# Optimization experiments

Hardware: AMD Instinct MI355X
Metric: run time of the kernel (lower is better)

The kernel has to match this reference:

```python
import jax, jax.numpy as jnp
import numpy as np

B, S, D, H = 2, 2048, 1024, 16
DK = D // H


def setup_inputs() -> dict:
    key = jax.random.key(0)
    ks = jax.random.split(key, 7)
    q = jax.random.normal(ks[0], (B, S, D), dtype=jnp.float32)
    k = jax.random.normal(ks[1], (B, S, D), dtype=jnp.float32)
    v = jax.random.normal(ks[2], (B, S, D), dtype=jnp.float32)
    # causal mask: mask==0 positions get -1e9 before softmax
    mask = jnp.tril(jnp.ones((S, S), dtype=jnp.int32))[None, None, :, :]
    scale = 0.02
    w_q = jax.random.normal(ks[3], (D, D), dtype=jnp.float32) * scale
    w_k = jax.random.normal(ks[4], (D, D), dtype=jnp.float32) * scale
    w_v = jax.random.normal(ks[5], (D, D), dtype=jnp.float32) * scale
    w_o = jax.random.normal(ks[6], (D, D), dtype=jnp.float32) * scale
    return {"q": q, "k": k, "v": v, "mask": mask,
            "w_q": w_q, "w_k": w_k, "w_v": w_v, "w_o": w_o}


def reference(q, k, v, mask, w_q, w_k, w_v, w_o):
    # nn.Linear(bias=False): x @ W.T
    query = q @ w_q.T  # [B,S,D]
    key = k @ w_k.T
    value = v @ w_v.T
    # split heads -> [B,H,S,DK]
    query = query.reshape(B, S, H, DK).transpose(0, 2, 1, 3)
    key = key.reshape(B, S, H, DK).transpose(0, 2, 1, 3)
    value = value.reshape(B, S, H, DK).transpose(0, 2, 1, 3)
    scores = jnp.einsum('bhqd,bhkd->bhqk', query, key) / jnp.sqrt(
        jnp.asarray(DK, dtype=query.dtype))
    scores = jnp.where(mask == 0, jnp.asarray(-1e9, scores.dtype), scores)
    attn = jax.nn.softmax(scores, axis=-1)  # dropout p=0.0 -> identity
    x = jnp.einsum('bhqk,bhkd->bhqd', attn, value)  # [B,H,S,DK]
    x = x.transpose(0, 2, 1, 3).reshape(B, S, D)
    return x @ w_o.T
```

## Files before the change

### kernel.cpp

```cpp
#include <hip/hip_runtime.h>

typedef __attribute__((ext_vector_type(8))) short short8;
typedef __attribute__((ext_vector_type(4))) float f32x4;

#define DEVI static __device__ __forceinline__

constexpr int BB = 2, SS = 2048, DD = 1024, HH = 16, DKK = 64;
constexpr size_t QN = (size_t)BB * SS * DD;
constexpr size_t WN = (size_t)DD * DD;

constexpr size_t OFF_WQ = 3 * QN;
constexpr size_t OFF_WO = OFF_WQ + 3 * WN;
constexpr size_t OFF_QM = OFF_WQ + 4 * WN;
constexpr size_t OFF_KM = OFF_QM + QN;
constexpr size_t OFF_VM = OFF_QM + 2 * QN;
constexpr size_t OFF_XC = OFF_QM + 3 * QN;

DEVI unsigned short f2bf(float f) {
  unsigned int u = __float_as_uint(f);
  u = (u + 0x7fffu + ((u >> 16) & 1u)) >> 16;
  return (unsigned short)u;
}

DEVI f32x4 fzero() { f32x4 z = {0.f, 0.f, 0.f, 0.f}; return z; }

DEVI void gld16(const void* g, void* l) {
  __builtin_amdgcn_global_load_lds((__attribute__((address_space(1))) void*)g,
                                   (__attribute__((address_space(3))) void*)l,
                                   16, 0, 0);
}

DEVI short8 mk8u(unsigned int a, unsigned int b, unsigned int c, unsigned int d) {
  union { short8 s; unsigned int u[4]; } x;
  x.u[0] = a; x.u[1] = b; x.u[2] = c; x.u[3] = d;
  return x.s;
}

DEVI short8 mk8q(unsigned long long lo, unsigned long long hi) {
  union { short8 s; unsigned long long q[2]; } x;
  x.q[0] = lo; x.q[1] = hi;
  return x.s;
}

DEVI unsigned int pkbf(float a, float b) {
  return __builtin_amdgcn_perm(__float_as_uint(b), __float_as_uint(a), 0x07060302u);
}

#define VMBAR(N) asm volatile("s_waitcnt vmcnt(" #N ")\n\ts_barrier" ::: "memory")
#define LGKM0                                      \
  do {                                             \
    asm volatile("s_waitcnt lgkmcnt(0)" ::: "memory"); \
    __builtin_amdgcn_sched_barrier(0);             \
  } while (0)

__global__ __launch_bounds__(256) void convert_all(
    const float* __restrict__ q, const float* __restrict__ k,
    const float* __restrict__ v, const float* __restrict__ wq,
    const float* __restrict__ wk, const float* __restrict__ wv,
    const float* __restrict__ wo, unsigned short* __restrict__ ws) {
  size_t t = (size_t)blockIdx.x * 256 + threadIdx.x;
  size_t e = t * 4;
  const float* src;
  size_t base, idx;
  if (e < 3 * QN) {
    size_t a = e >> 22;
    idx = e & (QN - 1);
    src = (a == 0) ? q : (a == 1) ? k : v;
    base = a * QN;
  } else {
    size_t r = e - 3 * QN;
    size_t a = r >> 20;
    idx = r & (WN - 1);
    src = (a == 0) ? wq : (a == 1) ? wk : (a == 2) ? wv : wo;
    base = 3 * QN + a * WN;
  }
  float4 f = *(const float4*)(src + idx);
  ushort4 o;
  o.x = f2bf(f.x); o.y = f2bf(f.y); o.z = f2bf(f.z); o.w = f2bf(f.w);
  *(ushort4*)(ws + base + idx) = o;
}

__global__ __launch_bounds__(512, 2) void proj_gemm(unsigned short* __restrict__ ws) {
  __shared__ unsigned short lds[65536];
  const int tid = threadIdx.x;
  const int w = tid >> 6, l = tid & 63;
  const int lr = l & 15, qd = l >> 4, l7 = l & 7, l3 = l >> 3;
  const int wr = w >> 2, wc = w & 3;

  const int orig = blockIdx.x;
  const int swz = (orig & 7) * 24 + (orig >> 3);
  const int mt = swz >> 2, nt = swz & 3;
  const int z = mt >> 4;
  const int m0 = (mt & 15) * 256, n0 = nt * 256;

  const unsigned short* Ab = ws + (size_t)z * QN;
  const unsigned short* Wb = ws + OFF_WQ + (size_t)z * WN;
  unsigned short* O = ws + OFF_QM + (size_t)z * QN;

  f32x4 acc[8][4];
#pragma unroll
  for (int i = 0; i < 8; ++i)
#pragma unroll
    for (int j = 0; j < 4; ++j) acc[i][j] = fzero();

  auto stage = [&](int buf, int ab, int h, int kt) {
    const unsigned short* src = ab ? Wb : Ab;
    const int rc0 = (ab ? n0 : m0) + h * 128 + w * 8 + l3;
    const int kofs = kt * 64 + ((l7 ^ l3) * 8);
    unsigned short* d = &lds[buf * 32768 + ab * 16384 + h * 8192 + w * 512];
#pragma unroll
    for (int u = 0; u < 2; ++u)
      gld16(src + (size_t)(rc0 + u * 64) * DD + kofs, d + u * 4096);
  };
  auto rdA = [&](int buf, int fi, int ks) -> short8 {
    const int rg = (fi * 2 + wr) * 16 + lr;
    const int c2 = (ks * 4 + qd) ^ l7;
    return *(const short8*)&lds[buf * 32768 + rg * 64 + c2 * 8];
  };
  auto rdB = [&](int buf, int fj, int ks) -> short8 {
    const int rg = (fj * 4 + wc) * 16 + lr;
    const int c2 = (ks * 4 + qd) ^ l7;
    return *(const short8*)&lds[buf * 32768 + 16384 + rg * 64 + c2 * 8];
  };

  stage(0, 0, 0, 0);
  stage(0, 1, 0, 0);
  stage(0, 1, 1, 0);
  stage(0, 0, 1, 0);

  constexpr int NT = DD / 64;
#pragma unroll 1
  for (int t = 0; t < NT; ++t) {
    const int rb = t & 1, wb = rb ^ 1;
    const bool g = (t + 1 < NT);
    short8 af[4][2], bf[2][2], bh[2][2];

    VMBAR(4);
    if (g) stage(wb, 0, 0, t + 1);
#pragma unroll
    for (int mi = 0; mi < 4; ++mi)
#pragma unroll
      for (int ks = 0; ks < 2; ++ks) af[mi][ks] = rdA(rb, mi, ks);
#pragma unroll
    for (int nj = 0; nj < 2; ++nj)
#pragma unroll
      for (int ks = 0; ks < 2; ++ks) bf[nj][ks] = rdB(rb, nj, ks);
    LGKM0;
    __builtin_amdgcn_s_setprio(1);
#pragma unroll
    for (int mi = 0; mi < 4; ++mi)
#pragma unroll
      for (int nj = 0; nj < 2; ++nj)
#pragma unroll
        for (int ks = 0; ks < 2; ++ks)
          acc[mi][nj] = __builtin_amdgcn_mfma_f32_16x16x32_bf16(
              af[mi][ks], bf[nj][ks], acc[mi][nj], 0, 0, 0);
    __builtin_amdgcn_s_setprio(0);

    if (g) { VMBAR(4); } else { VMBAR(2); }
    if (g) stage(wb, 1, 0, t + 1);
#pragma unroll
    for (int nj = 0; nj < 2; ++nj)
#pragma unroll
      for (int ks = 0; ks < 2; ++ks) bh[nj][ks] = rdB(rb, 2 + nj, ks);
    LGKM0;
    __builtin_amdgcn_s_setprio(1);
#pragma unroll
    for (int mi = 0; mi < 4; ++mi)
#pragma unroll
      for (int nj = 0; nj < 2; ++nj)
#pragma unroll
        for (int ks = 0; ks < 2; ++ks)
          acc[mi][2 + nj] = __builtin_amdgcn_mfma_f32_16x16x32_bf16(
              af[mi][ks], bh[nj][ks], acc[mi][2 + nj], 0, 0, 0);
    __builtin_amdgcn_s_setprio(0);

    if (g) { VMBAR(4); } else { VMBAR(0); }
    if (g) stage(wb, 1, 1, t + 1);
#pragma unroll
    for (int mi = 0; mi < 4; ++mi)
#pragma unroll
      for (int ks = 0; ks < 2; ++ks) af[mi][ks] = rdA(rb, 4 + mi, ks);
    LGKM0;
    __builtin_amdgcn_s_setprio(1);
#pragma unroll
    for (int mi = 0; mi < 4; ++mi)
#pragma unroll
      for (int nj = 0; nj < 2; ++nj)
#pragma unroll
        for (int ks = 0; ks < 2; ++ks)
          acc[4 + mi][nj] = __builtin_amdgcn_mfma_f32_16x16x32_bf16(
              af[mi][ks], bf[nj][ks], acc[4 + mi][nj], 0, 0, 0);
    __builtin_amdgcn_s_setprio(0);

    if (g) stage(wb, 0, 1, t + 1);
    __builtin_amdgcn_s_setprio(1);
#pragma unroll
    for (int mi = 0; mi < 4; ++mi)
#pragma unroll
      for (int nj = 0; nj < 2; ++nj)
#pragma unroll
        for (int ks = 0; ks < 2; ++ks)
          acc[4 + mi][2 + nj] = __builtin_amdgcn_mfma_f32_16x16x32_bf16(
              af[mi][ks], bh[nj][ks], acc[4 + mi][2 + nj], 0, 0, 0);
    __builtin_amdgcn_s_setprio(0);
  }

  if (z == 2) {
#pragma unroll
    for (int fi = 0; fi < 8; ++fi)
#pragma unroll
      for (int fj = 0; fj < 4; ++fj) {
        const int n = n0 + (fj * 4 + wc) * 16 + lr;
        const int h = n >> 6, dk = n & 63;
        const int m = m0 + (fi * 2 + wr) * 16 + qd * 4;
        const int b = m >> 11, s = m & 2047;
        ushort4 pk;
        pk.x = f2bf(acc[fi][fj][0]); pk.y = f2bf(acc[fi][fj][1]);
        pk.z = f2bf(acc[fi][fj][2]); pk.w = f2bf(acc[fi][fj][3]);
        *(ushort4*)&O[((size_t)(b * HH + h) * DKK + dk) * SS + s] = pk;
      }
  } else {
#pragma unroll
    for (int fi = 0; fi < 8; ++fi)
#pragma unroll
      for (int fj = 0; fj < 4; ++fj) {
        const int n = n0 + (fj * 4 + wc) * 16 + lr;
        const int h = n >> 6, dk = n & 63;
#pragma unroll
        for (int i = 0; i < 4; ++i) {
          const int m = m0 + (fi * 2 + wr) * 16 + qd * 4 + i;
          const int b = m >> 11, s = m & 2047;
          O[((size_t)(b * HH + h) * SS + s) * DKK + dk] = f2bf(acc[fi][fj][i]);
        }
      }
  }
}

DEVI void gemm64_db(const unsigned short* __restrict__ A,
                    const unsigned short* __restrict__ Bw,
                    unsigned short* ldsA, unsigned short* ldsB,
                    int m0, int n0, f32x4 acc[4][2]) {
  const int tid = threadIdx.x;
  const int w = tid >> 6, l = tid & 63;
  const int lr = l & 15, qd = l >> 4;

#pragma unroll
  for (int i = 0; i < 4; ++i)
#pragma unroll
    for (int j = 0; j < 2; ++j) acc[i][j] = fzero();

  const unsigned short* pa[2];
  const unsigned short* pb[4];
  int lsa[2], lsb[4];
#pragma unroll
  for (int kh = 0; kh < 2; ++kh) {
    pa[kh] = A + (size_t)(m0 + w * 16 + lr) * DD + kh * 32 + qd * 8;
    lsa[kh] = (w * 2 + kh) * 512;
  }
#pragma unroll
  for (int r = 0; r < 2; ++r)
#pragma unroll
    for (int kh = 0; kh < 2; ++kh) {
      pb[r * 2 + kh] = Bw + (size_t)(n0 + (2 * w + r) * 16 + lr) * DD + kh * 32 + qd * 8;
      lsb[r * 2 + kh] = ((2 * w + r) * 2 + kh) * 512;
    }

#pragma unroll
  for (int u = 0; u < 2; ++u) gld16(pa[u], ldsA + lsa[u]);
#pragma unroll
  for (int u = 0; u < 4; ++u) gld16(pb[u], ldsB + lsb[u]);

  constexpr int NIT = DD / 64;
#pragma unroll 1
  for (int it = 0; it < NIT; ++it) {
    __syncthreads();
    const int curA = (it & 1) * 4096, curB = (it & 1) * 8192;
    if (it + 1 < NIT) {
      const int k1 = (it + 1) * 64;
      const int nxtA = 4096 - curA, nxtB = 8192 - curB;
#pragma unroll
      for (int u = 0; u < 2; ++u) gld16(pa[u] + k1, ldsA + nxtA + lsa[u]);
#pragma unroll
      for (int u = 0; u < 4; ++u) gld16(pb[u] + k1, ldsB + nxtB + lsb[u]);
    }
#pragma unroll
    for (int ks = 0; ks < 2; ++ks) {
      short8 af[4], bf[2];
#pragma unroll
      for (int im = 0; im < 4; ++im)
        af[im] = *(const short8*)&ldsA[curA + (im * 2 + ks) * 512 + l * 8];
#pragma unroll
      for (int in = 0; in < 2; ++in)
        bf[in] = *(const short8*)&ldsB[curB + ((2 * w + in) * 2 + ks) * 512 + l * 8];
#pragma unroll
      for (int im = 0; im < 4; ++im)
#pragma unroll
        for (int in = 0; in < 2; ++in)
          acc[im][in] = __builtin_amdgcn_mfma_f32_16x16x32_bf16(
              af[im], bf[in], acc[im][in], 0, 0, 0);
    }
  }
}

__global__ __launch_bounds__(512) void flash_attn(
    const unsigned short* __restrict__ Qm, const unsigned short* __restrict__ Km,
    const unsigned short* __restrict__ Vt, unsigned short* __restrict__ Xc) {
  __shared__ unsigned short Kl[2][4096];
  __shared__ unsigned short Vl[2][4096];
  const int head = blockIdx.x, py = blockIdx.y, b = blockIdx.z;
  const int p = b ? 15 - py : py;
  const int tid = threadIdx.x, w = tid >> 6, l = tid & 63, lr = l & 15, qd = l >> 4;
  const int slr = lr ^ ((lr >> 3) << 2);
  const size_t bh = (size_t)(b * HH + head);
  const unsigned short* Qb = Qm + bh * SS * DKK;
  const unsigned short* Kb = Km + bh * SS * DKK;
  const unsigned short* Vb = Vt + bh * DKK * SS;

  const bool heavy = (w < 4);
  const int qt = heavy ? (31 - p) : p;
  const int nkv = 32 - p;
  const int qrow = qt * 64 + (w & 3) * 16 + lr;

  const int s0 = heavy ? w : (w - 4);
  const int s1 = s0 + 4;
  const int loOff = ((qd >> 1) * 16 + slr) * 8 + (qd & 1) * 4;
  const int hiOff = ((2 + (qd >> 1)) * 16 + slr) * 8 + (qd & 1) * 4;

  short8 qf0 = *(const short8*)&Qb[(size_t)qrow * DKK + qd * 8];
  short8 qf1 = *(const short8*)&Qb[(size_t)qrow * DKK + 32 + qd * 8];

  f32x4 o[4];
#pragma unroll
  for (int i = 0; i < 4; ++i) o[i] = fzero();
  float ll = 0.f;
  const float c1 = 0.18033688011112042f;
  const float mc = 8.0f * c1;

  {
    if (heavy) {
      gld16(&Kb[(size_t)((s0 >> 1) * 16 + lr) * DKK + (s0 & 1) * 32 + qd * 8],
            &Kl[0][s0 * 512]);
      gld16(&Kb[(size_t)((s1 >> 1) * 16 + lr) * DKK + (s1 & 1) * 32 + qd * 8],
            &Kl[0][s1 * 512]);
    } else {
      gld16(&Vb[(size_t)((s0 >> 1) * 16 + slr) * SS + (s0 & 1) * 32 + qd * 8],
            &Vl[0][s0 * 512]);
      gld16(&Vb[(size_t)((s1 >> 1) * 16 + slr) * SS + (s1 & 1) * 32 + qd * 8],
            &Vl[0][s1 * 512]);
    }
  }

#pragma unroll 1
  for (int kv = 0; kv < nkv; ++kv) {
    __syncthreads();
    const int cur = kv & 1;
    if (kv + 1 < nkv) {
      const int kv0n = (kv + 1) * 64;
      if (heavy) {
        gld16(&Kb[(size_t)(kv0n + (s0 >> 1) * 16 + lr) * DKK + (s0 & 1) * 32 + qd * 8],
              &Kl[cur ^ 1][s0 * 512]);
        gld16(&Kb[(size_t)(kv0n + (s1 >> 1) * 16 + lr) * DKK + (s1 & 1) * 32 + qd * 8],
              &Kl[cur ^ 1][s1 * 512]);
      } else {
        gld16(&Vb[(size_t)((s0 >> 1) * 16 + slr) * SS + kv0n + (s0 & 1) * 32 + qd * 8],
              &Vl[cur ^ 1][s0 * 512]);
        gld16(&Vb[(size_t)((s1 >> 1) * 16 + slr) * SS + kv0n + (s1 & 1) * 32 + qd * 8],
              &Vl[cur ^ 1][s1 * 512]);
      }
    }

    if (kv <= qt) {
      const int kv0 = kv * 64;
      f32x4 sc[4];
#pragma unroll
      for (int nt = 0; nt < 4; ++nt) {
        short8 kf0 = *(const short8*)&Kl[cur][(nt * 2 + 0) * 512 + l * 8];
        short8 kf1 = *(const short8*)&Kl[cur][(nt * 2 + 1) * 512 + l * 8];
        f32x4 zz = fzero();
        zz = __builtin_amdgcn_mfma_f32_16x16x32_bf16(kf0, qf0, zz, 0, 0, 0);
        sc[nt] = __builtin_amdgcn_mfma_f32_16x16x32_bf16(kf1, qf1, zz, 0, 0, 0);
      }
      if (kv == qt) {
#pragma unroll
        for (int nt = 0; nt < 4; ++nt)
#pragma unroll
          for (int i = 0; i < 4; ++i) {
            const int kvi = kv0 + nt * 16 + qd * 4 + i;
            if (kvi > qrow) sc[nt][i] = -3e38f;
          }
      }

      float rs = 0.f;
#pragma unroll
      for (int nt = 0; nt < 4; ++nt)
#pragma unroll
        for (int i = 0; i < 4; ++i) {
          const float pp = exp2f(fmaf(sc[nt][i], c1, -mc));
          sc[nt][i] = pp;
          rs += pp;
        }
      rs += __shfl_xor(rs, 16);
      rs += __shfl_xor(rs, 32);
      ll += rs;

      unsigned int pd[4][2];
#pragma unroll
      for (int f = 0; f < 4; ++f) {
        pd[f][0] = pkbf(sc[f][0], sc[f][1]);
        pd[f][1] = pkbf(sc[f][2], sc[f][3]);
      }

#pragma unroll
      for (int kh = 0; kh < 2; ++kh) {
        short8 bfr = mk8u(pd[2 * kh][0], pd[2 * kh][1],
                          pd[2 * kh + 1][0], pd[2 * kh + 1][1]);
#pragma unroll
        for (int mt = 0; mt < 4; ++mt) {
          const int sbase = (mt * 2 + kh) * 512;
          const unsigned long long lo =
              *(const unsigned long long*)&Vl[cur][sbase + loOff];
          const unsigned long long hi =
              *(const unsigned long long*)&Vl[cur][sbase + hiOff];
          o[mt] = __builtin_amdgcn_mfma_f32_16x16x32_bf16(mk8q(lo, hi), bfr,
                                                          o[mt], 0, 0, 0);
        }
      }
    }
  }

  const float inv = 1.0f / ll;
  unsigned short* Xr = Xc + ((size_t)b * SS + qrow) * DD + (size_t)head * DKK;
#pragma unroll
  for (int mt = 0; mt < 4; ++mt)
#pragma unroll
    for (int i = 0; i < 4; ++i)
      Xr[mt * 16 + qd * 4 + i] = f2bf(o[mt][i] * inv);
}

__global__ __launch_bounds__(256) void out_gemm(
    const unsigned short* __restrict__ Xc, const unsigned short* __restrict__ Wo,
    float* __restrict__ out) {
  __shared__ unsigned short ldsA[8192];
  __shared__ unsigned short ldsB[16384];
  const int m0 = blockIdx.x * 64, n0 = blockIdx.y * 128;
  f32x4 acc[4][2];
  gemm64_db(Xc, Wo, ldsA, ldsB, m0, n0, acc);

  const int tid = threadIdx.x;
  const int w = tid >> 6, l = tid & 63, lr = l & 15, qd = l >> 4;
#pragma unroll
  for (int im = 0; im < 4; ++im)
#pragma unroll
    for (int in = 0; in < 2; ++in) {
      const int n = n0 + w * 32 + in * 16 + lr;
#pragma unroll
      for (int i = 0; i < 4; ++i) {
        const int m = m0 + im * 16 + qd * 4 + i;
        out[(size_t)m * DD + n] = acc[im][in][i];
      }
    }
}

extern "C" void kernel_launch(void* const* d_in, const int* in_sizes, int n_in,
                              void* d_out, int out_size, void* d_ws, size_t ws_size,
                              hipStream_t stream) {
  (void)in_sizes; (void)n_in; (void)out_size; (void)ws_size;
  const float* q  = (const float*)d_in[0];
  const float* k  = (const float*)d_in[1];
  const float* v  = (const float*)d_in[2];
  const float* wq = (const float*)d_in[4];
  const float* wk = (const float*)d_in[5];
  const float* wv = (const float*)d_in[6];
  const float* wo = (const float*)d_in[7];
  unsigned short* ws = (unsigned short*)d_ws;
  float* out = (float*)d_out;

  convert_all<<<dim3(16384), dim3(256), 0, stream>>>(q, k, v, wq, wk, wv, wo, ws);
  proj_gemm<<<dim3(192), dim3(512), 0, stream>>>(ws);
  flash_attn<<<dim3(16, 16, 2), dim3(512), 0, stream>>>(ws + OFF_QM, ws + OFF_KM,
                                                        ws + OFF_VM, ws + OFF_XC);
  out_gemm<<<dim3(64, 8), dim3(256), 0, stream>>>(ws + OFF_XC, ws + OFF_WO, out);
}
```

Before: 227.9 us.

## Simplify flash attention to one q-tile per block; retile output GEMM 128x128

Flash attention drops the heavy/light wave-pair scheme. Each 256-thread block now handles one query tile, loading both K and V per step, and the grid grows to 32 query tiles ordered to interleave heavy and light causal work. The output projection GEMM moves from 64x128 to 128x128 tiles with XOR-swizzled LDS, staged loads interleaved with MFMA phases, and priority hints. This aims to raise MFMA reuse and occupancy, at the cost of less intra-block load balancing and larger register and LDS use per block.

```diff
diff --git a/kernel.cpp b/kernel.cpp
--- a/kernel.cpp
+++ b/kernel.cpp
@@ -237,79 +237,13 @@
   }
 }
 
-DEVI void gemm64_db(const unsigned short* __restrict__ A,
-                    const unsigned short* __restrict__ Bw,
-                    unsigned short* ldsA, unsigned short* ldsB,
-                    int m0, int n0, f32x4 acc[4][2]) {
-  const int tid = threadIdx.x;
-  const int w = tid >> 6, l = tid & 63;
-  const int lr = l & 15, qd = l >> 4;
-
-#pragma unroll
-  for (int i = 0; i < 4; ++i)
-#pragma unroll
-    for (int j = 0; j < 2; ++j) acc[i][j] = fzero();
-
-  const unsigned short* pa[2];
-  const unsigned short* pb[4];
-  int lsa[2], lsb[4];
-#pragma unroll
-  for (int kh = 0; kh < 2; ++kh) {
-    pa[kh] = A + (size_t)(m0 + w * 16 + lr) * DD + kh * 32 + qd * 8;
-    lsa[kh] = (w * 2 + kh) * 512;
-  }
-#pragma unroll
-  for (int r = 0; r < 2; ++r)
-#pragma unroll
-    for (int kh = 0; kh < 2; ++kh) {
-      pb[r * 2 + kh] = Bw + (size_t)(n0 + (2 * w + r) * 16 + lr) * DD + kh * 32 + qd * 8;
-      lsb[r * 2 + kh] = ((2 * w + r) * 2 + kh) * 512;
-    }
-
-#pragma unroll
-  for (int u = 0; u < 2; ++u) gld16(pa[u], ldsA + lsa[u]);
-#pragma unroll
-  for (int u = 0; u < 4; ++u) gld16(pb[u], ldsB + lsb[u]);
-
-  constexpr int NIT = DD / 64;
-#pragma unroll 1
-  for (int it = 0; it < NIT; ++it) {
-    __syncthreads();
-    const int curA = (it & 1) * 4096, curB = (it & 1) * 8192;
-    if (it + 1 < NIT) {
-      const int k1 = (it + 1) * 64;
-      const int nxtA = 4096 - curA, nxtB = 8192 - curB;
-#pragma unroll
-      for (int u = 0; u < 2; ++u) gld16(pa[u] + k1, ldsA + nxtA + lsa[u]);
-#pragma unroll
-      for (int u = 0; u < 4; ++u) gld16(pb[u] + k1, ldsB + nxtB + lsb[u]);
-    }
-#pragma unroll
-    for (int ks = 0; ks < 2; ++ks) {
-      short8 af[4], bf[2];
-#pragma unroll
-      for (int im = 0; im < 4; ++im)
-        af[im] = *(const short8*)&ldsA[curA + (im * 2 + ks) * 512 + l * 8];
-#pragma unroll
-      for (int in = 0; in < 2; ++in)
-        bf[in] = *(const short8*)&ldsB[curB + ((2 * w + in) * 2 + ks) * 512 + l * 8];
-#pragma unroll
-      for (int im = 0; im < 4; ++im)
-#pragma unroll
-        for (int in = 0; in < 2; ++in)
-          acc[im][in] = __builtin_amdgcn_mfma_f32_16x16x32_bf16(
-              af[im], bf[in], acc[im][in], 0, 0, 0);
-    }
-  }
-}
-
-__global__ __launch_bounds__(512) void flash_attn(
+__global__ __launch_bounds__(256) void flash_attn(
     const unsigned short* __restrict__ Qm, const unsigned short* __restrict__ Km,
     const unsigned short* __restrict__ Vt, unsigned short* __restrict__ Xc) {
   __shared__ unsigned short Kl[2][4096];
   __shared__ unsigned short Vl[2][4096];
-  const int head = blockIdx.x, py = blockIdx.y, b = blockIdx.z;
-  const int p = b ? 15 - py : py;
+  const int head = blockIdx.x, qy = blockIdx.y, b = blockIdx.z;
+  const int qt = (qy < 16) ? qy : 47 - qy;
   const int tid = threadIdx.x, w = tid >> 6, l = tid & 63, lr = l & 15, qd = l >> 4;
   const int slr = lr ^ ((lr >> 3) << 2);
   const size_t bh = (size_t)(b * HH + head);
@@ -317,13 +251,19 @@
   const unsigned short* Kb = Km + bh * SS * DKK;
   const unsigned short* Vb = Vt + bh * DKK * SS;
 
-  const bool heavy = (w < 4);
-  const int qt = heavy ? (31 - p) : p;
-  const int nkv = 32 - p;
-  const int qrow = qt * 64 + (w & 3) * 16 + lr;
-
-  const int s0 = heavy ? w : (w - 4);
-  const int s1 = s0 + 4;
+  const int nkv = qt + 1;
+  const int qrow = qt * 64 + w * 16 + lr;
+
+  const int s0 = w, s1 = w + 4;
+  const unsigned short* kb0 =
+      &Kb[(size_t)((s0 >> 1) * 16 + lr) * DKK + (s0 & 1) * 32 + qd * 8];
+  const unsigned short* kb1 =
+      &Kb[(size_t)((s1 >> 1) * 16 + lr) * DKK + (s1 & 1) * 32 + qd * 8];
+  const unsigned short* vb0 =
+      &Vb[(size_t)((s0 >> 1) * 16 + slr) * SS + (s0 & 1) * 32 + qd * 8];
+  const unsigned short* vb1 =
+      &Vb[(size_t)((s1 >> 1) * 16 + slr) * SS + (s1 & 1) * 32 + qd * 8];
+
   const int loOff = ((qd >> 1) * 16 + slr) * 8 + (qd & 1) * 4;
   const int hiOff = ((2 + (qd >> 1)) * 16 + slr) * 8 + (qd & 1) * 4;
 
@@ -338,17 +278,10 @@
   const float mc = 8.0f * c1;
 
   {
-    if (heavy) {
-      gld16(&Kb[(size_t)((s0 >> 1) * 16 + lr) * DKK + (s0 & 1) * 32 + qd * 8],
-            &Kl[0][s0 * 512]);
-      gld16(&Kb[(size_t)((s1 >> 1) * 16 + lr) * DKK + (s1 & 1) * 32 + qd * 8],
-            &Kl[0][s1 * 512]);
-    } else {
-      gld16(&Vb[(size_t)((s0 >> 1) * 16 + slr) * SS + (s0 & 1) * 32 + qd * 8],
-            &Vl[0][s0 * 512]);
-      gld16(&Vb[(size_t)((s1 >> 1) * 16 + slr) * SS + (s1 & 1) * 32 + qd * 8],
-            &Vl[0][s1 * 512]);
-    }
+    gld16(kb0, &Kl[0][s0 * 512]);
+    gld16(kb1, &Kl[0][s1 * 512]);
+    gld16(vb0, &Vl[0][s0 * 512]);
+    gld16(vb1, &Vl[0][s1 * 512]);
   }
 
 #pragma unroll 1
@@ -356,21 +289,15 @@
     __syncthreads();
     const int cur = kv & 1;
     if (kv + 1 < nkv) {
-      const int kv0n = (kv + 1) * 64;
-      if (heavy) {
-        gld16(&Kb[(size_t)(kv0n + (s0 >> 1) * 16 + lr) * DKK + (s0 & 1) * 32 + qd * 8],
-              &Kl[cur ^ 1][s0 * 512]);
-        gld16(&Kb[(size_t)(kv0n + (s1 >> 1) * 16 + lr) * DKK + (s1 & 1) * 32 + qd * 8],
-              &Kl[cur ^ 1][s1 * 512]);
-      } else {
-        gld16(&Vb[(size_t)((s0 >> 1) * 16 + slr) * SS + kv0n + (s0 & 1) * 32 + qd * 8],
-              &Vl[cur ^ 1][s0 * 512]);
-        gld16(&Vb[(size_t)((s1 >> 1) * 16 + slr) * SS + kv0n + (s1 & 1) * 32 + qd * 8],
-              &Vl[cur ^ 1][s1 * 512]);
-      }
+      const size_t koff = (size_t)(kv + 1) * (64 * DKK);
+      const size_t voff = (size_t)(kv + 1) * 64;
+      gld16(kb0 + koff, &Kl[cur ^ 1][s0 * 512]);
+      gld16(kb1 + koff, &Kl[cur ^ 1][s1 * 512]);
+      gld16(vb0 + voff, &Vl[cur ^ 1][s0 * 512]);
+      gld16(vb1 + voff, &Vl[cur ^ 1][s1 * 512]);
     }
 
-    if (kv <= qt) {
+    {
       const int kv0 = kv * 64;
       f32x4 sc[4];
 #pragma unroll
@@ -438,26 +365,134 @@
       Xr[mt * 16 + qd * 4 + i] = f2bf(o[mt][i] * inv);
 }
 
-__global__ __launch_bounds__(256) void out_gemm(
+__global__ __launch_bounds__(256, 2) void out_gemm(
     const unsigned short* __restrict__ Xc, const unsigned short* __restrict__ Wo,
     float* __restrict__ out) {
-  __shared__ unsigned short ldsA[8192];
-  __shared__ unsigned short ldsB[16384];
-  const int m0 = blockIdx.x * 64, n0 = blockIdx.y * 128;
-  f32x4 acc[4][2];
-  gemm64_db(Xc, Wo, ldsA, ldsB, m0, n0, acc);
-
+  __shared__ unsigned short lds[32768];
   const int tid = threadIdx.x;
-  const int w = tid >> 6, l = tid & 63, lr = l & 15, qd = l >> 4;
-#pragma unroll
-  for (int im = 0; im < 4; ++im)
-#pragma unroll
-    for (int in = 0; in < 2; ++in) {
-      const int n = n0 + w * 32 + in * 16 + lr;
+  const int w = tid >> 6, l = tid & 63;
+  const int lr = l & 15, qd = l >> 4, l7 = l & 7, l3 = l >> 3;
+  const int wr = w >> 1, wc = w & 1;
+  const int m0 = blockIdx.x * 128, n0 = blockIdx.y * 128;
+
+  f32x4 acc[4][4];
+#pragma unroll
+  for (int i = 0; i < 4; ++i)
+#pragma unroll
+    for (int j = 0; j < 4; ++j) acc[i][j] = fzero();
+
+  auto stage = [&](int buf, int ab, int h, int kt) {
+    const unsigned short* src = ab ? Wo : Xc;
+    const int rc0 = (ab ? n0 : m0) + h * 64 + w * 8 + l3;
+    const int kofs = kt * 64 + ((l7 ^ l3) * 8);
+    unsigned short* d = &lds[buf * 16384 + ab * 8192 + h * 4096 + w * 512];
+#pragma unroll
+    for (int u = 0; u < 2; ++u)
+      gld16(src + (size_t)(rc0 + u * 32) * DD + kofs, d + u * 2048);
+  };
+  auto rdA = [&](int buf, int mf, int ks) -> short8 {
+    const int rg = mf * 16 + lr;
+    const int c2 = (ks * 4 + qd) ^ l7;
+    return *(const short8*)&lds[buf * 16384 + rg * 64 + c2 * 8];
+  };
+  auto rdB = [&](int buf, int nf, int ks) -> short8 {
+    const int rg = nf * 16 + lr;
+    const int c2 = (ks * 4 + qd) ^ l7;
+    return *(const short8*)&lds[buf * 16384 + 8192 + rg * 64 + c2 * 8];
+  };
+
+  stage(0, 0, 0, 0);
+  stage(0, 1, 0, 0);
+  stage(0, 1, 1, 0);
+  stage(0, 0, 1, 0);
+
+  constexpr int NT = DD / 64;
+#pragma unroll 1
+  for (int t = 0; t < NT; ++t) {
+    const int rb = t & 1, wb = rb ^ 1;
+    const bool g = (t + 1 < NT);
+    short8 af[2][2], bf[2][2], bh[2][2];
+
+    VMBAR(4);
+    if (g) stage(wb, 0, 0, t + 1);
+#pragma unroll
+    for (int mi = 0; mi < 2; ++mi)
+#pragma unroll
+      for (int ks = 0; ks < 2; ++ks) af[mi][ks] = rdA(rb, mi * 2 + wr, ks);
+#pragma unroll
+    for (int nj = 0; nj < 2; ++nj)
+#pragma unroll
+      for (int ks = 0; ks < 2; ++ks) bf[nj][ks] = rdB(rb, nj * 2 + wc, ks);
+    LGKM0;
+    __builtin_amdgcn_s_setprio(1);
+#pragma unroll
+    for (int mi = 0; mi < 2; ++mi)
+#pragma unroll
+      for (int nj = 0; nj < 2; ++nj)
+#pragma unroll
+        for (int ks = 0; ks < 2; ++ks)
+          acc[mi][nj] = __builtin_amdgcn_mfma_f32_16x16x32_bf16(
+              af[mi][ks], bf[nj][ks], acc[mi][nj], 0, 0, 0);
+    __builtin_amdgcn_s_setprio(0);
+
+    if (g) { VMBAR(4); } else { VMBAR(2); }
+    if (g) stage(wb, 1, 0, t + 1);
+#pragma unroll
+    for (int nj = 0; nj < 2; ++nj)
+#pragma unroll
+      for (int ks = 0; ks < 2; ++ks) bh[nj][ks] = rdB(rb, (2 + nj) * 2 + wc, ks);
+    LGKM0;
+    __builtin_amdgcn_s_setprio(1);
+#pragma unroll
+    for (int mi = 0; mi < 2; ++mi)
+#pragma unroll
+      for (int nj = 0; nj < 2; ++nj)
+#pragma unroll
+        for (int ks = 0; ks < 2; ++ks)
+          acc[mi][2 + nj] = __builtin_amdgcn_mfma_f32_16x16x32_bf16(
+              af[mi][ks], bh[nj][ks], acc[mi][2 + nj], 0, 0, 0);
+    __builtin_amdgcn_s_setprio(0);
+
+    if (g) { VMBAR(4); } else { VMBAR(0); }
+    if (g) stage(wb, 1, 1, t + 1);
+#pragma unroll
+    for (int mi = 0; mi < 2; ++mi)
+#pragma unroll
+      for (int ks = 0; ks < 2; ++ks) af[mi][ks] = rdA(rb, (2 + mi) * 2 + wr, ks);
+    LGKM0;
+    __builtin_amdgcn_s_setprio(1);
+#pragma unroll
+    for (int mi = 0; mi < 2; ++mi)
+#pragma unroll
+      for (int nj = 0; nj < 2; ++nj)
+#pragma unroll
+        for (int ks = 0; ks < 2; ++ks)
+          acc[2 + mi][nj] = __builtin_amdgcn_mfma_f32_16x16x32_bf16(
+              af[mi][ks], bf[nj][ks], acc[2 + mi][nj], 0, 0, 0);
+    __builtin_amdgcn_s_setprio(0);
+
+    if (g) stage(wb, 0, 1, t + 1);
+    __builtin_amdgcn_s_setprio(1);
+#pragma unroll
+    for (int mi = 0; mi < 2; ++mi)
+#pragma unroll
+      for (int nj = 0; nj < 2; ++nj)
+#pragma unroll
+        for (int ks = 0; ks < 2; ++ks)
+          acc[2 + mi][2 + nj] = __builtin_amdgcn_mfma_f32_16x16x32_bf16(
+              af[mi][ks], bh[nj][ks], acc[2 + mi][2 + nj], 0, 0, 0);
+    __builtin_amdgcn_s_setprio(0);
+  }
+
+#pragma unroll
+  for (int a = 0; a < 4; ++a)
+#pragma unroll
+    for (int c = 0; c < 4; ++c) {
+      const int n = n0 + (c * 2 + wc) * 16 + lr;
 #pragma unroll
       for (int i = 0; i < 4; ++i) {
-        const int m = m0 + im * 16 + qd * 4 + i;
-        out[(size_t)m * DD + n] = acc[im][in][i];
+        const int m = m0 + (a * 2 + wr) * 16 + qd * 4 + i;
+        out[(size_t)m * DD + n] = acc[a][c][i];
       }
     }
 }
@@ -478,7 +513,7 @@
 
   convert_all<<<dim3(16384), dim3(256), 0, stream>>>(q, k, v, wq, wk, wv, wo, ws);
   proj_gemm<<<dim3(192), dim3(512), 0, stream>>>(ws);
-  flash_attn<<<dim3(16, 16, 2), dim3(512), 0, stream>>>(ws + OFF_QM, ws + OFF_KM,
+  flash_attn<<<dim3(16, 32, 2), dim3(256), 0, stream>>>(ws + OFF_QM, ws + OFF_KM,
                                                         ws + OFF_VM, ws + OFF_XC);
-  out_gemm<<<dim3(64, 8), dim3(256), 0, stream>>>(ws + OFF_XC, ws + OFF_WO, out);
-}
+  out_gemm<<<dim3(32, 8), dim3(256), 0, stream>>>(ws + OFF_XC, ws + OFF_WO, out);
+}
```

Result: no change. 227.6 us (-0.1%).
